# Performance work log

Measured on AMD Instinct MI355X. Metric: run time of the kernel, lower is better.

The kernel has to match this reference:

```python
import jax, jax.numpy as jnp
import numpy as np

B, N, C, OUT = 4, 512, 128, 128

def setup_inputs() -> dict:
    key = jax.random.key(0)
    k1, k2, k3 = jax.random.split(key, 3)
    adj_matrix = jax.random.bernoulli(k1, 0.1, (B, N, N)).astype(jnp.float32)
    features = jax.random.normal(k2, (B, N, C), dtype=jnp.float32)
    # xavier_uniform for Linear(2C -> OUT): weight stored here as [2C, OUT]
    limit = float(np.sqrt(6.0 / (2 * C + OUT)))
    W = jax.random.uniform(k3, (2 * C, OUT), minval=-limit, maxval=limit, dtype=jnp.float32)
    b = jnp.zeros((OUT,), dtype=jnp.float32)
    return {"adj_matrix": adj_matrix, "features": features, "W": W, "b": b}

def reference(adj_matrix, features, W, b):
    # pooling aggregator: masked max over neighbors (materializes [B,N,N,C], as in source)
    neg_inf = jnp.finfo(features.dtype).min
    mask = (adj_matrix > 0)[..., None]                      # [B,N,N,1]
    feat_nb = jnp.where(mask, features[:, None, :, :], neg_inf)  # [B,N,N,C]
    agg = jnp.max(feat_nb, axis=2)                          # [B,N,C]
    agg = jnp.where(jnp.isfinite(agg), agg, 0.0)
    neigh = jax.nn.relu(agg)
    combined = jnp.concatenate([features, neigh], axis=-1)  # [B,N,2C]
    return jnp.einsum('bnc,co->bno', combined, W) + b       # [B,N,OUT]
```

## Files before the change

### kernel.cpp

```cpp
#include <hip/hip_runtime.h>
#include <hip/hip_bf16.h>
#include <float.h>


#define Bsz 4
#define Nn  512
#define Cc  128
#define OUTn 128
#define NNODES (Bsz * Nn)
#define KK (2 * Cc)

typedef __bf16 bf16x8 __attribute__((ext_vector_type(8)));
typedef float  f32x4  __attribute__((ext_vector_type(4)));

static __device__ __forceinline__ unsigned short f2bf(float x) {
    __hip_bfloat16 h = __float2bfloat16(x);
    return *reinterpret_cast<unsigned short*>(&h);
}

__global__ __launch_bounds__(256) void prep_wt(
    const float* __restrict__ W, unsigned short* __restrict__ Wt)
{
    int idx = blockIdx.x * 256 + threadIdx.x;
    int kk = idx >> 7;
    int n  = idx & 127;
    float v = W[idx];
    Wt[n * KK + kk] = f2bf(v);
}

__global__ __launch_bounds__(256) void sage_agg(
    const float* __restrict__ adj,
    const float* __restrict__ feat,
    unsigned short* __restrict__ comb)
{
    const int w = threadIdx.x >> 6;
    const int l = threadIdx.x & 63;
    const int node = blockIdx.x * 4 + w;
    const int b = node >> 9;
    const int i = node & (Nn - 1);

    __shared__ unsigned short nbr[4][Nn];

    const float* adjrow = adj + (size_t)node * Nn;
    const float2* f2 = (const float2*)(feat + (size_t)b * Nn * Cc);

    int cnt = 0;
    #pragma unroll
    for (int ch = 0; ch < Nn / 64; ++ch) {
        float a = adjrow[ch * 64 + l];
        unsigned long long mask = __ballot(a > 0.0f);
        int pos = __popcll(mask & ((1ull << l) - 1ull));
        if (a > 0.0f) nbr[w][cnt + pos] = (unsigned short)(ch * 64 + l);
        cnt += __popcll(mask);
    }
    __syncthreads();

    float m0 = -FLT_MAX, m1 = -FLT_MAX;
    int k = 0;
    for (; k + 4 <= cnt; k += 4) {
        int j0 = nbr[w][k + 0], j1 = nbr[w][k + 1];
        int j2 = nbr[w][k + 2], j3 = nbr[w][k + 3];
        float2 v0 = f2[j0 * 64 + l];
        float2 v1 = f2[j1 * 64 + l];
        float2 v2 = f2[j2 * 64 + l];
        float2 v3 = f2[j3 * 64 + l];
        m0 = fmaxf(m0, fmaxf(fmaxf(v0.x, v1.x), fmaxf(v2.x, v3.x)));
        m1 = fmaxf(m1, fmaxf(fmaxf(v0.y, v1.y), fmaxf(v2.y, v3.y)));
    }
    for (; k < cnt; ++k) {
        int j = nbr[w][k];
        float2 v = f2[j * 64 + l];
        m0 = fmaxf(m0, v.x);
        m1 = fmaxf(m1, v.y);
    }

    float n0 = fmaxf(m0, 0.0f), n1 = fmaxf(m1, 0.0f);
    float2 s = f2[i * 64 + l];

    ushort2* crow = (ushort2*)(comb + (size_t)node * KK);
    ushort2 sv; sv.x = f2bf(s.x); sv.y = f2bf(s.y);
    ushort2 nv; nv.x = f2bf(n0);  nv.y = f2bf(n1);
    crow[l]      = sv;
    crow[64 + l] = nv;
}

__global__ __launch_bounds__(256) void sage_gemm(
    const __bf16* __restrict__ A,
    const __bf16* __restrict__ Bt,
    const float* __restrict__ bias,
    float* __restrict__ out)
{
    const int wave = threadIdx.x >> 6;
    const int lane = threadIdx.x & 63;
    const int tile = blockIdx.x * 4 + wave;
    const int nt = tile & 7;
    const int mt = tile >> 3;

    const int frow = lane & 15;
    const int koff = (lane >> 4) * 8;

    const __bf16* pa = A  + (size_t)(mt * 16 + frow) * KK + koff;
    const __bf16* pb = Bt + (size_t)(nt * 16 + frow) * KK + koff;

    f32x4 acc = {0.f, 0.f, 0.f, 0.f};
    #pragma unroll
    for (int ks = 0; ks < KK / 32; ++ks) {
        bf16x8 af = *(const bf16x8*)(pa + ks * 32);
        bf16x8 bf = *(const bf16x8*)(pb + ks * 32);
        acc = __builtin_amdgcn_mfma_f32_16x16x32_bf16(af, bf, acc, 0, 0, 0);
    }

    const int col = lane & 15;
    const int r0  = (lane >> 4) * 4;
    const float bv = bias[nt * 16 + col];
    #pragma unroll
    for (int r = 0; r < 4; ++r) {
        out[(size_t)(mt * 16 + r0 + r) * OUTn + nt * 16 + col] = acc[r] + bv;
    }
}

extern "C" void kernel_launch(void* const* d_in, const int* in_sizes, int n_in,
                              void* d_out, int out_size, void* d_ws, size_t ws_size,
                              hipStream_t stream) {
    const float* adj  = (const float*)d_in[0];
    const float* feat = (const float*)d_in[1];
    const float* W    = (const float*)d_in[2];
    const float* bias = (const float*)d_in[3];
    float* out = (float*)d_out;

    unsigned short* comb = (unsigned short*)d_ws;
    unsigned short* Wt   = comb + (size_t)NNODES * KK;

    prep_wt  <<<dim3(KK * OUTn / 256), dim3(256), 0, stream>>>(W, Wt);
    sage_agg <<<dim3(NNODES / 4),      dim3(256), 0, stream>>>(adj, feat, comb);
    sage_gemm<<<dim3(NNODES / 16 * (OUTn / 16) / 4), dim3(256), 0, stream>>>(
        (const __bf16*)comb, (const __bf16*)Wt, bias, out);
}
```

Before: 73.57 us.

## Split neighbor aggregation across four waves per node and drop weight prep kernel

The aggregation kernel now gives each node a whole block: each of four waves scans a quarter of the adjacency row, builds a local neighbor list and takes a partial max. The partial maxima are combined through shared memory by one wave, which then writes the bf16 combined row. Separately, the weight transpose/convert kernel is removed and the GEMM reads fp32 W directly with strided scalar loads, converting to bf16 in registers. This removes a kernel launch and adds parallelism to the latency-bound gather, at the cost of uncoalesced W loads in the GEMM.

```diff
diff --git a/kernel.cpp b/kernel.cpp
--- a/kernel.cpp
+++ b/kernel.cpp
@@ -17,15 +17,9 @@
     __hip_bfloat16 h = __float2bfloat16(x);
     return *reinterpret_cast<unsigned short*>(&h);
 }
-
-__global__ __launch_bounds__(256) void prep_wt(
-    const float* __restrict__ W, unsigned short* __restrict__ Wt)
-{
-    int idx = blockIdx.x * 256 + threadIdx.x;
-    int kk = idx >> 7;
-    int n  = idx & 127;
-    float v = W[idx];
-    Wt[n * KK + kk] = f2bf(v);
+static __device__ __forceinline__ __bf16 f2bf16(float x) {
+    unsigned short u = f2bf(x);
+    return *reinterpret_cast<__bf16*>(&u);
 }
 
 __global__ __launch_bounds__(256) void sage_agg(
@@ -35,25 +29,26 @@
 {
     const int w = threadIdx.x >> 6;
     const int l = threadIdx.x & 63;
-    const int node = blockIdx.x * 4 + w;
+    const int node = blockIdx.x;
     const int b = node >> 9;
     const int i = node & (Nn - 1);
 
-    __shared__ unsigned short nbr[4][Nn];
+    __shared__ unsigned short nbr[4][128];
+    __shared__ float2 pmax[4][64];
 
     const float* adjrow = adj + (size_t)node * Nn;
     const float2* f2 = (const float2*)(feat + (size_t)b * Nn * Cc);
 
     int cnt = 0;
     #pragma unroll
-    for (int ch = 0; ch < Nn / 64; ++ch) {
-        float a = adjrow[ch * 64 + l];
+    for (int ch = 0; ch < 2; ++ch) {
+        int j = w * 128 + ch * 64 + l;
+        float a = adjrow[j];
         unsigned long long mask = __ballot(a > 0.0f);
         int pos = __popcll(mask & ((1ull << l) - 1ull));
-        if (a > 0.0f) nbr[w][cnt + pos] = (unsigned short)(ch * 64 + l);
+        if (a > 0.0f) nbr[w][cnt + pos] = (unsigned short)j;
         cnt += __popcll(mask);
     }
-    __syncthreads();
 
     float m0 = -FLT_MAX, m1 = -FLT_MAX;
     int k = 0;
@@ -73,20 +68,28 @@
         m0 = fmaxf(m0, v.x);
         m1 = fmaxf(m1, v.y);
     }
+    pmax[w][l] = make_float2(m0, m1);
+    __syncthreads();
 
-    float n0 = fmaxf(m0, 0.0f), n1 = fmaxf(m1, 0.0f);
-    float2 s = f2[i * 64 + l];
+    if (w == 0) {
+        float2 p0 = pmax[0][l], p1 = pmax[1][l], p2 = pmax[2][l], p3 = pmax[3][l];
+        float n0 = fmaxf(fmaxf(p0.x, p1.x), fmaxf(p2.x, p3.x));
+        float n1 = fmaxf(fmaxf(p0.y, p1.y), fmaxf(p2.y, p3.y));
+        n0 = fmaxf(n0, 0.0f);
+        n1 = fmaxf(n1, 0.0f);
+        float2 s = f2[i * 64 + l];
 
-    ushort2* crow = (ushort2*)(comb + (size_t)node * KK);
-    ushort2 sv; sv.x = f2bf(s.x); sv.y = f2bf(s.y);
-    ushort2 nv; nv.x = f2bf(n0);  nv.y = f2bf(n1);
-    crow[l]      = sv;
-    crow[64 + l] = nv;
+        ushort2* crow = (ushort2*)(comb + (size_t)node * KK);
+        ushort2 sv; sv.x = f2bf(s.x); sv.y = f2bf(s.y);
+        ushort2 nv; nv.x = f2bf(n0);  nv.y = f2bf(n1);
+        crow[l]      = sv;
+        crow[64 + l] = nv;
+    }
 }
 
 __global__ __launch_bounds__(256) void sage_gemm(
     const __bf16* __restrict__ A,
-    const __bf16* __restrict__ Bt,
+    const float* __restrict__ W,
     const float* __restrict__ bias,
     float* __restrict__ out)
 {
@@ -99,14 +102,18 @@
     const int frow = lane & 15;
     const int koff = (lane >> 4) * 8;
 
-    const __bf16* pa = A  + (size_t)(mt * 16 + frow) * KK + koff;
-    const __bf16* pb = Bt + (size_t)(nt * 16 + frow) * KK + koff;
+    const __bf16* pa = A + (size_t)(mt * 16 + frow) * KK + koff;
+    const float*  wp = W + nt * 16 + frow;
 
     f32x4 acc = {0.f, 0.f, 0.f, 0.f};
     #pragma unroll
     for (int ks = 0; ks < KK / 32; ++ks) {
         bf16x8 af = *(const bf16x8*)(pa + ks * 32);
-        bf16x8 bf = *(const bf16x8*)(pb + ks * 32);
+        bf16x8 bf;
+        #pragma unroll
+        for (int j = 0; j < 8; ++j) {
+            bf[j] = f2bf16(wp[(size_t)(ks * 32 + koff + j) * OUTn]);
+        }
         acc = __builtin_amdgcn_mfma_f32_16x16x32_bf16(af, bf, acc, 0, 0, 0);
     }
 
@@ -129,10 +136,8 @@
     float* out = (float*)d_out;
 
     unsigned short* comb = (unsigned short*)d_ws;
-    unsigned short* Wt   = comb + (size_t)NNODES * KK;
 
-    prep_wt  <<<dim3(KK * OUTn / 256), dim3(256), 0, stream>>>(W, Wt);
-    sage_agg <<<dim3(NNODES / 4),      dim3(256), 0, stream>>>(adj, feat, comb);
+    sage_agg <<<dim3(NNODES), dim3(256), 0, stream>>>(adj, feat, comb);
     sage_gemm<<<dim3(NNODES / 16 * (OUTn / 16) / 4), dim3(256), 0, stream>>>(
-        (const __bf16*)comb, (const __bf16*)Wt, bias, out);
+        (const __bf16*)comb, W, bias, out);
 }
```

After: 68.53 us. 6.9% less time.
